# Optimization experiments

Measured on AMD Instinct MI355X. Metric: run time of the kernel, lower is better.

Reference implementation:

```python
import jax, jax.numpy as jnp
import numpy as np

N = 100000   # nodes
E = 1000000  # edges
IN, H, OUT = 256, 64, 16


def setup_inputs() -> dict:
    key = jax.random.key(0)
    k0, k1, k2, k3 = jax.random.split(key, 4)
    x = jax.random.normal(k0, (N, IN), jnp.float32)
    edge_index = jax.random.randint(k1, (2, E), 0, N)
    # GCNConv parameters (glorot-ish weights, zero bias as in PyG defaults)
    W1 = jax.random.normal(k2, (IN, H), jnp.float32) / np.sqrt(IN).astype(np.float32)
    b1 = jnp.zeros((H,), jnp.float32)
    W2 = jax.random.normal(k3, (H, OUT), jnp.float32) / np.sqrt(H).astype(np.float32)
    b2 = jnp.zeros((OUT,), jnp.float32)
    return {"x": x, "edge_index": edge_index, "W1": W1, "b1": b1, "W2": W2, "b2": b2}


def gcn_conv(x, W, b, src, dst, n):
    # PyG GCNConv: h = x @ W; out[v] = sum_{(u->v)} norm(u,v) * h[u] + b
    h = x @ W                                    # [n, out]
    deg = jnp.zeros((n,), h.dtype).at[dst].add(1.0)
    dinv = jnp.where(deg > 0, jax.lax.rsqrt(deg), 0.0)
    norm = dinv[src] * dinv[dst]                 # [E+n] symmetric normalization
    msg = h[src] * norm[:, None]                 # gather + scale
    agg = jax.ops.segment_sum(msg, dst, num_segments=n)  # scatter-add
    return agg + b


def reference(x, edge_index, W1, b1, W2, b2):
    n = x.shape[0]
    # add self-loops (PyG GCNConv default add_self_loops=True)
    loops = jnp.arange(n, dtype=edge_index.dtype)
    src = jnp.concatenate([edge_index[0], loops])
    dst = jnp.concatenate([edge_index[1], loops])
    h = gcn_conv(x, W1, b1, src, dst, n)
    h = jax.nn.relu(h)  # F.dropout is identity in eval mode (training=False)
    return gcn_conv(h, W2, b2, src, dst, n)
```

## Files before the change

### kernel.cpp

```cpp
#include <hip/hip_runtime.h>

namespace {
constexpr int NN  = 100000;
constexpr int NE  = 1000000;
constexpr int INF = 256;
constexpr int HF  = 64;
constexpr int OF  = 16;
constexpr int SCAN_CHUNK = 1024;
constexpr int NBLK = (NN + SCAN_CHUNK - 1) / SCAN_CHUNK;
constexpr int NSEG = 8;
constexpr int SEGW = (NN + NSEG - 1) / NSEG;
constexpr int CNTW = 100096;
constexpr int ZBLK = (CNTW / 4 + 255) / 256;
constexpr int GB   = (NN + 127) / 128;
constexpr int ECHUNK = 2048;
constexpr int EGRP = (NE + ECHUNK - 1) / ECHUNK;
constexpr int SB   = EGRP * NSEG;
}

typedef __attribute__((ext_vector_type(8))) short     sh8;
typedef __attribute__((ext_vector_type(4))) float     f32x4;
typedef __attribute__((ext_vector_type(8))) unsigned short us8;

__device__ __forceinline__ unsigned short f2bf(float f) {
    unsigned int u = __builtin_bit_cast(unsigned int, f);
    u += 0x7FFFu + ((u >> 16) & 1u);
    return (unsigned short)(u >> 16);
}
__device__ __forceinline__ float bf2f(unsigned short s) {
    return __builtin_bit_cast(float, (unsigned int)s << 16);
}

__global__ void k_pre(int* __restrict__ cnt, const float* __restrict__ W1,
                      unsigned short* __restrict__ wt_g) {
    int b = blockIdx.x, t = threadIdx.x;
    if (b < ZBLK) {
        int i = (b * 256 + t) * 4;
        if (i < CNTW) *(int4*)(cnt + i) = (int4){0, 0, 0, 0};
    } else {
        int idx = (b - ZBLK) * 256 + t;
        int c = idx >> 8, k = idx & 255;
        wt_g[idx] = f2bf(W1[(size_t)k * HF + c]);
    }
}

__global__ __launch_bounds__(256) void k_hist(const int* __restrict__ dst,
                                              int* __restrict__ cnt) {
    int b   = blockIdx.x;
    int seg = b & (NSEG - 1);
    int grp = b >> 3;
    int e0  = grp * ECHUNK + threadIdx.x;
    int d[8];
    #pragma unroll
    for (int i = 0; i < 8; ++i) {
        int e = e0 + i * 256;
        d[i] = (e < NE) ? dst[e] : -1;
    }
    #pragma unroll
    for (int i = 0; i < 8; ++i) {
        if ((unsigned)d[i] / (unsigned)SEGW == (unsigned)seg)
            atomicAdd(&cnt[d[i]], 1);
    }
}

__global__ __launch_bounds__(256) void k_reduce(const int* __restrict__ cnt,
                                                int* __restrict__ bsum,
                                                float* __restrict__ dinv) {
    int t = threadIdx.x;
    int i0 = blockIdx.x * SCAN_CHUNK + t * 4;
    int s = 0;
    float dv[4] = {0.f, 0.f, 0.f, 0.f};
    #pragma unroll
    for (int q = 0; q < 4; ++q) {
        if (i0 + q < NN) {
            int c = cnt[i0 + q];
            s += c;
            dv[q] = rsqrtf((float)(c + 1));
        }
    }
    if (i0 + 3 < NN) *(float4*)(dinv + i0) = (float4){dv[0], dv[1], dv[2], dv[3]};
    else { for (int q = 0; q < 4; ++q) if (i0 + q < NN) dinv[i0 + q] = dv[q]; }
    #pragma unroll
    for (int off = 32; off > 0; off >>= 1) s += __shfl_down(s, off);
    __shared__ int wsum[4];
    int lane = t & 63, wid = t >> 6;
    if (lane == 0) wsum[wid] = s;
    __syncthreads();
    if (t == 0) bsum[blockIdx.x] = wsum[0] + wsum[1] + wsum[2] + wsum[3];
}

__global__ __launch_bounds__(256) void k_scan(const int* __restrict__ cnt,
                                              const int* __restrict__ bsum,
                                              int* __restrict__ rowptr,
                                              int* __restrict__ cursor) {
    int t = threadIdx.x;
    int b = blockIdx.x;
    int lane = t & 63, wid = t >> 6;

    int p = 0;
    if (lane < b) p += bsum[lane];
    if (64 + lane < b) p += bsum[64 + lane];
    #pragma unroll
    for (int off = 32; off > 0; off >>= 1) p += __shfl_down(p, off);
    int blockBase = __shfl(p, 0);

    int i0 = b * SCAN_CHUNK + t * 4;
    int v0 = 0, v1 = 0, v2 = 0, v3 = 0;
    if (i0 + 0 < NN) v0 = cnt[i0 + 0];
    if (i0 + 1 < NN) v1 = cnt[i0 + 1];
    if (i0 + 2 < NN) v2 = cnt[i0 + 2];
    if (i0 + 3 < NN) v3 = cnt[i0 + 3];
    int tsum = v0 + v1 + v2 + v3;
    int incl = tsum;
    #pragma unroll
    for (int off = 1; off < 64; off <<= 1) {
        int n = __shfl_up(incl, off);
        if (lane >= off) incl += n;
    }
    __shared__ int wsum[4];
    if (lane == 63) wsum[wid] = incl;
    __syncthreads();
    int woff = 0;
    for (int w = 0; w < wid; ++w) woff += wsum[w];
    int excl = woff + (incl - tsum) + blockBase;
    int e0 = excl, e1 = e0 + v0, e2 = e1 + v1, e3 = e2 + v2;
    if (i0 + 0 < NN) { rowptr[i0 + 0] = e0; cursor[i0 + 0] = e0; }
    if (i0 + 1 < NN) { rowptr[i0 + 1] = e1; cursor[i0 + 1] = e1; }
    if (i0 + 2 < NN) { rowptr[i0 + 2] = e2; cursor[i0 + 2] = e2; }
    if (i0 + 3 < NN) { rowptr[i0 + 3] = e3; cursor[i0 + 3] = e3; }
    if (i0 + 3 == NN - 1) rowptr[NN] = e3 + v3;
}

__global__ __launch_bounds__(256, 4) void k_gs(const float* __restrict__ x,
                                               const unsigned short* __restrict__ wt_g,
                                               unsigned short* __restrict__ h1,
                                               const int* __restrict__ src,
                                               const int* __restrict__ dst,
                                               int* __restrict__ cursor,
                                               int* __restrict__ eidx) {
    __shared__ unsigned short wt[64 * 264];
    int b = blockIdx.x;
    int t = threadIdx.x;

    if (b >= GB) {
        int sb  = b - GB;
        int seg = sb & (NSEG - 1);
        int grp = sb >> 3;
        int e0  = grp * ECHUNK + t;
        int d[8];
        #pragma unroll
        for (int i = 0; i < 8; ++i) {
            int e = e0 + i * 256;
            d[i] = (e < NE) ? dst[e] : -1;
        }
        #pragma unroll
        for (int i = 0; i < 8; ++i) {
            if ((unsigned)d[i] / (unsigned)SEGW == (unsigned)seg) {
                int p = atomicAdd(&cursor[d[i]], 1);
                eidx[p] = src[e0 + i * 256];
            }
        }
        return;
    }

    int w = t >> 6, l = t & 63;
    int row0 = b * 128;

    #pragma unroll
    for (int p = 0; p < 8; ++p) {
        int T   = p * 256 + t;
        int c   = T >> 5;
        int kb8 = T & 31;
        *(us8*)(wt + c * 264 + kb8 * 8) = *(const us8*)(wt_g + c * 256 + kb8 * 8);
    }
    __syncthreads();

    int m = l & 15;
    int g = l >> 4;
    int gr0 = row0 + w * 32 + m;      if (gr0 > NN - 1) gr0 = NN - 1;
    int gr1 = row0 + w * 32 + 16 + m; if (gr1 > NN - 1) gr1 = NN - 1;
    const float* p0 = x + (size_t)gr0 * INF + g * 8;
    const float* p1 = x + (size_t)gr1 * INF + g * 8;

    f32x4 acc[2][4];
    #pragma unroll
    for (int i = 0; i < 2; ++i)
        #pragma unroll
        for (int j = 0; j < 4; ++j) acc[i][j] = (f32x4){0.f, 0.f, 0.f, 0.f};

    float4 u0 = *(const float4*)(p0);
    float4 u1 = *(const float4*)(p0 + 4);
    float4 u2 = *(const float4*)(p1);
    float4 u3 = *(const float4*)(p1 + 4);
    for (int kb = 0; kb < INF; kb += 32) {
        float4 v0 = u0, v1 = u1, v2 = u2, v3 = u3;
        if (kb + 32 < INF) {
            u0 = *(const float4*)(p0 + kb + 32);
            u1 = *(const float4*)(p0 + kb + 36);
            u2 = *(const float4*)(p1 + kb + 32);
            u3 = *(const float4*)(p1 + kb + 36);
        }
        us8 a0u = { f2bf(v0.x), f2bf(v0.y), f2bf(v0.z), f2bf(v0.w),
                    f2bf(v1.x), f2bf(v1.y), f2bf(v1.z), f2bf(v1.w) };
        us8 a1u = { f2bf(v2.x), f2bf(v2.y), f2bf(v2.z), f2bf(v2.w),
                    f2bf(v3.x), f2bf(v3.y), f2bf(v3.z), f2bf(v3.w) };
        sh8 a0 = __builtin_bit_cast(sh8, a0u);
        sh8 a1 = __builtin_bit_cast(sh8, a1u);
        #pragma unroll
        for (int nt = 0; nt < 4; ++nt) {
            sh8 bb = *(const sh8*)(wt + (nt * 16 + m) * 264 + kb + g * 8);
            acc[0][nt] = __builtin_amdgcn_mfma_f32_16x16x32_bf16(a0, bb, acc[0][nt], 0, 0, 0);
            acc[1][nt] = __builtin_amdgcn_mfma_f32_16x16x32_bf16(a1, bb, acc[1][nt], 0, 0, 0);
        }
    }

    #pragma unroll
    for (int mt = 0; mt < 2; ++mt) {
        #pragma unroll
        for (int r = 0; r < 4; ++r) {
            int gr = row0 + w * 32 + mt * 16 + (l >> 4) * 4 + r;
            if (gr < NN) {
                #pragma unroll
                for (int nt = 0; nt < 4; ++nt)
                    h1[(size_t)gr * HF + nt * 16 + (l & 15)] = f2bf(acc[mt][nt][r]);
            }
        }
    }
}

__global__ __launch_bounds__(256) void k_gather1(const int* __restrict__ rowptr,
                                                 const int* __restrict__ eidx,
                                                 const float* __restrict__ dinv,
                                                 const unsigned short* __restrict__ h1,
                                                 const float* __restrict__ b1,
                                                 const float* __restrict__ W2,
                                                 unsigned short* __restrict__ h2) {
    __shared__ float w2L[HF * OF];
    __shared__ float hrL[32][HF + 4];
    int t = threadIdx.x;
    *(float4*)(w2L + t * 4) = *(const float4*)(W2 + t * 4);

    int nodeL = t >> 3;
    int fg    = t & 7;
    int v     = blockIdx.x * 32 + nodeL;
    int beg = rowptr[v], end = rowptr[v + 1];

    float acc[8] = {};
    int   s_n = 0;  float w_n = 0.f;  us8 h_n = {};
    if (beg < end) {
        s_n = eidx[beg];
        w_n = dinv[s_n];
        h_n = *(const us8*)(h1 + (size_t)s_n * HF + fg * 8);
    }
    for (int i = beg; i < end; ++i) {
        float w_c = w_n;  us8 h_c = h_n;
        if (i + 1 < end) {
            s_n = eidx[i + 1];
            w_n = dinv[s_n];
            h_n = *(const us8*)(h1 + (size_t)s_n * HF + fg * 8);
        }
        #pragma unroll
        for (int q = 0; q < 8; ++q) acc[q] += w_c * bf2f(h_c[q]);
    }

    {
        float dv = dinv[v], sl = dv * dv;
        us8 hv = *(const us8*)(h1 + (size_t)v * HF + fg * 8);
        #pragma unroll
        for (int q = 0; q < 8; ++q) {
            float val = dv * acc[q] + sl * bf2f(hv[q]) + b1[fg * 8 + q];
            hrL[nodeL][fg * 8 + q] = val > 0.f ? val : 0.f;
        }
    }
    __syncthreads();

    #pragma unroll
    for (int T = t; T < 512; T += 256) {
        int n = T >> 4, j = T & 15;
        const float* hr = hrL[n];
        float p = 0.f;
        #pragma unroll
        for (int k = 0; k < HF; ++k) p += hr[k] * w2L[k * OF + j];
        h2[(size_t)(blockIdx.x * 32 + n) * OF + j] = f2bf(p);
    }
}

__global__ __launch_bounds__(256) void k_gather2(const int* __restrict__ rowptr,
                                                 const int* __restrict__ eidx,
                                                 const float* __restrict__ dinv,
                                                 const unsigned short* __restrict__ h2,
                                                 const float* __restrict__ b2,
                                                 float* __restrict__ out) {
    int t     = threadIdx.x;
    int nodeL = t >> 4;
    int j     = t & 15;
    int v     = blockIdx.x * 16 + nodeL;
    int beg = rowptr[v], end = rowptr[v + 1];

    float acc = 0.f;
    int   s_n = 0;  float w_n = 0.f;  unsigned short h_n = 0;
    if (beg < end) {
        s_n = eidx[beg];
        w_n = dinv[s_n];
        h_n = h2[(size_t)s_n * OF + j];
    }
    for (int i = beg; i < end; ++i) {
        float w_c = w_n;  unsigned short h_c = h_n;
        if (i + 1 < end) {
            s_n = eidx[i + 1];
            w_n = dinv[s_n];
            h_n = h2[(size_t)s_n * OF + j];
        }
        acc += w_c * bf2f(h_c);
    }
    float dv = dinv[v];
    out[(size_t)v * OF + j] = dv * acc + dv * dv * bf2f(h2[(size_t)v * OF + j]) + b2[j];
}

extern "C" void kernel_launch(void* const* d_in, const int* in_sizes, int n_in,
                              void* d_out, int out_size, void* d_ws, size_t ws_size,
                              hipStream_t stream) {
    const float* x   = (const float*)d_in[0];
    const int*   ei  = (const int*)d_in[1];
    const int*   src = ei;
    const int*   dst = ei + NE;
    const float* W1  = (const float*)d_in[2];
    const float* b1  = (const float*)d_in[3];
    const float* W2  = (const float*)d_in[4];
    const float* b2  = (const float*)d_in[5];
    float* out = (float*)d_out;

    float* dinv  = (float*)d_ws;
    unsigned short* h1b = (unsigned short*)(dinv + CNTW);
    unsigned short* h2b = (unsigned short*)(h1b + (size_t)NN * HF);
    int*   cnt   = (int*)(h2b + (size_t)NN * OF + (size_t)NN * OF);
    int*   rowptr = cnt + CNTW;
    int*   cursor = rowptr + 100352;
    int*   eidx  = cursor + CNTW;
    int*   bsum  = eidx + NE;
    unsigned short* wt_g = (unsigned short*)(bsum + 128);

    k_pre<<<ZBLK + 64, 256, 0, stream>>>(cnt, W1, wt_g);
    k_hist<<<SB, 256, 0, stream>>>(dst, cnt);
    k_reduce<<<NBLK, 256, 0, stream>>>(cnt, bsum, dinv);
    k_scan<<<NBLK, 256, 0, stream>>>(cnt, bsum, rowptr, cursor);

    k_gs<<<GB + SB, 256, 0, stream>>>(x, wt_g, h1b, src, dst, cursor, eidx);

    k_gather1<<<NN / 32, 256, 0, stream>>>(rowptr, eidx, dinv, h1b, b1, W2, h2b);

    k_gather2<<<NN / 16, 256, 0, stream>>>(rowptr, eidx, dinv, h2b, b2, out);
}
```

Before: 184.0 us.

## Halve GEMM weight LDS tile and raise k_gs occupancy to 8 blocks

The fused GEMM/scatter kernel now stages the transposed bf16 weight in two K-halves of 128 through a smaller LDS buffer (64x136 instead of 64x264). Launch bounds rise from 4 to 8 blocks per CU to allow more concurrent waves. The aim is higher occupancy to hide latency on the x stream. In exchange it adds an extra sync and reload phase per block and drops the explicit software prefetch of x, replacing it with a fully unrolled loop. The scatter blocks, which use no LDS, also benefit from the higher occupancy.

Result: faster. 180.3 us (-2.1%).

```diff
diff --git a/kernel.cpp b/kernel.cpp
--- a/kernel.cpp
+++ b/kernel.cpp
@@ -131,14 +131,14 @@
     if (i0 + 3 == NN - 1) rowptr[NN] = e3 + v3;
 }
 
-__global__ __launch_bounds__(256, 4) void k_gs(const float* __restrict__ x,
+__global__ __launch_bounds__(256, 8) void k_gs(const float* __restrict__ x,
                                                const unsigned short* __restrict__ wt_g,
                                                unsigned short* __restrict__ h1,
                                                const int* __restrict__ src,
                                                const int* __restrict__ dst,
                                                int* __restrict__ cursor,
                                                int* __restrict__ eidx) {
-    __shared__ unsigned short wt[64 * 264];
+    __shared__ unsigned short wt[64 * 136];
     int b = blockIdx.x;
     int t = threadIdx.x;
 
@@ -165,16 +165,6 @@
 
     int w = t >> 6, l = t & 63;
     int row0 = b * 128;
-
-    #pragma unroll
-    for (int p = 0; p < 8; ++p) {
-        int T   = p * 256 + t;
-        int c   = T >> 5;
-        int kb8 = T & 31;
-        *(us8*)(wt + c * 264 + kb8 * 8) = *(const us8*)(wt_g + c * 256 + kb8 * 8);
-    }
-    __syncthreads();
-
     int m = l & 15;
     int g = l >> 4;
     int gr0 = row0 + w * 32 + m;      if (gr0 > NN - 1) gr0 = NN - 1;
@@ -188,29 +178,37 @@
         #pragma unroll
         for (int j = 0; j < 4; ++j) acc[i][j] = (f32x4){0.f, 0.f, 0.f, 0.f};
 
-    float4 u0 = *(const float4*)(p0);
-    float4 u1 = *(const float4*)(p0 + 4);
-    float4 u2 = *(const float4*)(p1);
-    float4 u3 = *(const float4*)(p1 + 4);
-    for (int kb = 0; kb < INF; kb += 32) {
-        float4 v0 = u0, v1 = u1, v2 = u2, v3 = u3;
-        if (kb + 32 < INF) {
-            u0 = *(const float4*)(p0 + kb + 32);
-            u1 = *(const float4*)(p0 + kb + 36);
-            u2 = *(const float4*)(p1 + kb + 32);
-            u3 = *(const float4*)(p1 + kb + 36);
-        }
-        us8 a0u = { f2bf(v0.x), f2bf(v0.y), f2bf(v0.z), f2bf(v0.w),
-                    f2bf(v1.x), f2bf(v1.y), f2bf(v1.z), f2bf(v1.w) };
-        us8 a1u = { f2bf(v2.x), f2bf(v2.y), f2bf(v2.z), f2bf(v2.w),
-                    f2bf(v3.x), f2bf(v3.y), f2bf(v3.z), f2bf(v3.w) };
-        sh8 a0 = __builtin_bit_cast(sh8, a0u);
-        sh8 a1 = __builtin_bit_cast(sh8, a1u);
-        #pragma unroll
-        for (int nt = 0; nt < 4; ++nt) {
-            sh8 bb = *(const sh8*)(wt + (nt * 16 + m) * 264 + kb + g * 8);
-            acc[0][nt] = __builtin_amdgcn_mfma_f32_16x16x32_bf16(a0, bb, acc[0][nt], 0, 0, 0);
-            acc[1][nt] = __builtin_amdgcn_mfma_f32_16x16x32_bf16(a1, bb, acc[1][nt], 0, 0, 0);
+    #pragma unroll
+    for (int half = 0; half < 2; ++half) {
+        __syncthreads();
+        #pragma unroll
+        for (int p = 0; p < 4; ++p) {
+            int T   = p * 256 + t;
+            int c   = T >> 4;
+            int kb8 = T & 15;
+            *(us8*)(wt + c * 136 + kb8 * 8) =
+                *(const us8*)(wt_g + c * 256 + half * 128 + kb8 * 8);
+        }
+        __syncthreads();
+
+        #pragma unroll
+        for (int kb = 0; kb < 128; kb += 32) {
+            float4 u0 = *(const float4*)(p0 + half * 128 + kb);
+            float4 u1 = *(const float4*)(p0 + half * 128 + kb + 4);
+            float4 u2 = *(const float4*)(p1 + half * 128 + kb);
+            float4 u3 = *(const float4*)(p1 + half * 128 + kb + 4);
+            us8 a0u = { f2bf(u0.x), f2bf(u0.y), f2bf(u0.z), f2bf(u0.w),
+                        f2bf(u1.x), f2bf(u1.y), f2bf(u1.z), f2bf(u1.w) };
+            us8 a1u = { f2bf(u2.x), f2bf(u2.y), f2bf(u2.z), f2bf(u2.w),
+                        f2bf(u3.x), f2bf(u3.y), f2bf(u3.z), f2bf(u3.w) };
+            sh8 a0 = __builtin_bit_cast(sh8, a0u);
+            sh8 a1 = __builtin_bit_cast(sh8, a1u);
+            #pragma unroll
+            for (int nt = 0; nt < 4; ++nt) {
+                sh8 bb = *(const sh8*)(wt + (nt * 16 + m) * 136 + kb + g * 8);
+                acc[0][nt] = __builtin_amdgcn_mfma_f32_16x16x32_bf16(a0, bb, acc[0][nt], 0, 0, 0);
+                acc[1][nt] = __builtin_amdgcn_mfma_f32_16x16x32_bf16(a1, bb, acc[1][nt], 0, 0, 0);
+            }
         }
     }
 
```
